# Kernel tuning notes

Measured on AMD Instinct MI355X. Metric: run time of the kernel, lower is better.

## Reference

```python
import jax, jax.numpy as jnp
import numpy as np

N_NODES = 100000
N_EDGES = 1600000
IN_DIM, HIDDEN, OUT = 256, 128, 64


def setup_inputs() -> dict:
    key = jax.random.key(0)
    k1, k2, k3, k4 = jax.random.split(key, 4)
    x = jax.random.normal(k1, (N_NODES, IN_DIM), dtype=jnp.float32)
    edge_index = jax.random.randint(k2, (2, N_EDGES), 0, N_NODES, dtype=jnp.int32)
    # glorot-ish init for the GCN linear layers
    W1 = jax.random.normal(k3, (IN_DIM, HIDDEN), dtype=jnp.float32) / np.sqrt(IN_DIM)
    b1 = jnp.zeros((HIDDEN,), dtype=jnp.float32)
    W2 = jax.random.normal(k4, (HIDDEN, OUT), dtype=jnp.float32) / np.sqrt(HIDDEN)
    b2 = jnp.zeros((OUT,), dtype=jnp.float32)
    return {"x": x, "edge_index": edge_index, "W1": W1, "b1": b1, "W2": W2, "b2": b2}


def gcn_layer(x, src, dst, W, b):
    """PyG GCNConv: add self-loops, symmetric deg^-1/2 normalization,
    linear transform, scatter-add aggregation, bias."""
    h = x @ W  # [N, F_out]
    # degree over self-looped graph: in-degree(dst counts) + 1 self loop
    deg = jax.ops.segment_sum(jnp.ones((src.shape[0],), h.dtype), dst,
                              num_segments=N_NODES) + 1.0
    dinv = jax.lax.rsqrt(deg)  # [N]
    coef = dinv[src] * dinv[dst]  # [E]
    agg = jax.ops.segment_sum(h[src] * coef[:, None], dst, num_segments=N_NODES)
    # self-loop contribution (norm = dinv[i]^2) without materializing loop edges
    agg = agg + h * (dinv * dinv)[:, None]
    return agg + b


def reference(x, edge_index, W1, b1, W2, b2):
    src, dst = edge_index[0], edge_index[1]
    h = jax.nn.relu(gcn_layer(x, src, dst, W1, b1))
    return jax.nn.relu(gcn_layer(h, src, dst, W2, b2))
```

## Files before the change

### kernel.cpp

```cpp
#include <hip/hip_runtime.h>

#define N_NODES 100000
#define N_EDGES 1600000
#define IN_DIM 256
#define HIDDEN 128
#define OUT_DIM 64
#define LDA 40

#define NBIN 391
#define NBLK3 256
#define CHUNK 6250
#define NMAT (NBIN * NBLK3)
#define NBLK_SCAN (NMAT / 256)
#define CAP 6144

typedef __bf16 bf16x8 __attribute__((ext_vector_type(8)));
typedef __bf16 bf16x4 __attribute__((ext_vector_type(4)));
typedef float f32x4 __attribute__((ext_vector_type(4)));

__launch_bounds__(256)
__global__ void k_hist(const int* __restrict__ dst, int* __restrict__ cnt2) {
    __shared__ int hist[NBIN];
    for (int i = threadIdx.x; i < NBIN; i += 256) hist[i] = 0;
    __syncthreads();
    int base = blockIdx.x * CHUNK;
    for (int i = threadIdx.x; i < CHUNK; i += 256)
        atomicAdd(&hist[dst[base + i] >> 8], 1);
    __syncthreads();
    for (int k = threadIdx.x; k < NBIN; k += 256)
        cnt2[k * NBLK3 + blockIdx.x] = hist[k];
}

__global__ void k_scan1(int* __restrict__ a, int* __restrict__ bsum) {
    __shared__ int tmp[256];
    int t = threadIdx.x;
    int i = blockIdx.x * 256 + t;
    int v = a[i];
    tmp[t] = v;
    __syncthreads();
    #pragma unroll
    for (int off = 1; off < 256; off <<= 1) {
        int p = (t >= off) ? tmp[t - off] : 0;
        __syncthreads();
        tmp[t] += p;
        __syncthreads();
    }
    a[i] = tmp[t] - v;
    if (t == 255) bsum[blockIdx.x] = tmp[255];
}

__global__ void k_scan2(int* __restrict__ bsum) {
    __shared__ int tmp[512];
    int t = threadIdx.x;
    int v = (t < NBLK_SCAN) ? bsum[t] : 0;
    tmp[t] = v;
    __syncthreads();
    #pragma unroll
    for (int off = 1; off < 512; off <<= 1) {
        int p = (t >= off) ? tmp[t - off] : 0;
        __syncthreads();
        tmp[t] += p;
        __syncthreads();
    }
    if (t < NBLK_SCAN) bsum[t] = tmp[t] - v;
}

__global__ void k_scan3(int* __restrict__ a, const int* __restrict__ bsum) {
    int i = blockIdx.x * 256 + threadIdx.x;
    a[i] += bsum[blockIdx.x];
}

__launch_bounds__(256)
__global__ void k_scatter_bins(const int* __restrict__ src, const int* __restrict__ dst,
                               const int* __restrict__ off2,
                               unsigned int* __restrict__ ebuf) {
    __shared__ int cursor[NBIN];
    for (int k = threadIdx.x; k < NBIN; k += 256)
        cursor[k] = off2[k * NBLK3 + blockIdx.x];
    __syncthreads();
    int base = blockIdx.x * CHUNK;
    for (int i = threadIdx.x; i < CHUNK; i += 256) {
        int s = src[base + i], d = dst[base + i];
        int pos = atomicAdd(&cursor[d >> 8], 1);
        ebuf[pos] = ((unsigned)s << 8) | (unsigned)(d & 255);
    }
}

__launch_bounds__(256)
__global__ void k_fine(const unsigned int* __restrict__ ebuf, const int* __restrict__ off2,
                       int* __restrict__ esrc, int* __restrict__ rowstart,
                       float* __restrict__ dinv) {
    __shared__ int hist[256];
    __shared__ int tmp[256];
    __shared__ int nodeoff[256];
    __shared__ int cursor[256];
    __shared__ unsigned int ed[CAP];
    __shared__ int sOut[CAP];

    const int k = blockIdx.x;
    const int t = threadIdx.x;
    const int e0 = off2[k * NBLK3];
    const int e1 = (k + 1 < NBIN) ? off2[(k + 1) * NBLK3] : N_EDGES;
    int m = e1 - e0;
    if (m > CAP) m = CAP;

    hist[t] = 0;
    __syncthreads();
    for (int i = t; i < m; i += 256) {
        unsigned v = ebuf[e0 + i];
        ed[i] = v;
        atomicAdd(&hist[v & 255], 1);
    }
    __syncthreads();

    int v = hist[t];
    tmp[t] = v;
    __syncthreads();
    #pragma unroll
    for (int off = 1; off < 256; off <<= 1) {
        int p = (t >= off) ? tmp[t - off] : 0;
        __syncthreads();
        tmp[t] += p;
        __syncthreads();
    }
    nodeoff[t] = tmp[t] - v;
    cursor[t] = tmp[t] - v;
    __syncthreads();

    for (int i = t; i < m; i += 256) {
        unsigned e = ed[i];
        int pos = atomicAdd(&cursor[e & 255], 1);
        sOut[pos] = (int)(e >> 8);
    }
    __syncthreads();

    for (int i = t; i < m; i += 256) esrc[e0 + i] = sOut[i];

    int n = k * 256 + t;
    if (n < N_NODES) {
        rowstart[n] = e0 + nodeoff[t];
        dinv[n] = rsqrtf((float)hist[t] + 1.0f);
    }
    if (k == 0 && t == 0) rowstart[N_NODES] = N_EDGES;
}

__launch_bounds__(256, 2)
__global__ void k_gemm1(const float* __restrict__ X, const float* __restrict__ W1,
                        __bf16* __restrict__ H) {
    __shared__ __attribute__((aligned(16))) __bf16 As[128 * LDA];
    __shared__ __attribute__((aligned(16))) __bf16 Bs[128 * LDA];

    const int t = threadIdx.x;
    const int wave = t >> 6;
    const int lane = t & 63;
    const int wr = wave >> 1, wc = wave & 1;
    const int lm = lane & 15;
    const int q = lane >> 4;
    const int row0 = blockIdx.x * 128;

    f32x4 acc[4][4] = {};

    for (int k0 = 0; k0 < IN_DIM; k0 += 32) {
        #pragma unroll
        for (int p = 0; p < 4; ++p) {
            int r = p * 32 + (t >> 3);
            int kk = (t & 7) * 4;
            int g = row0 + r;
            float4 v = make_float4(0.f, 0.f, 0.f, 0.f);
            if (g < N_NODES) v = *(const float4*)&X[g * IN_DIM + k0 + kk];
            __bf16* dp = &As[r * LDA + kk];
            dp[0] = (__bf16)v.x; dp[1] = (__bf16)v.y;
            dp[2] = (__bf16)v.z; dp[3] = (__bf16)v.w;
        }
        #pragma unroll
        for (int p = 0; p < 4; ++p) {
            int idx = p * 256 + t;
            int kk = idx >> 5;
            int c = (idx & 31) * 4;
            float4 v = *(const float4*)&W1[(k0 + kk) * HIDDEN + c];
            Bs[(c + 0) * LDA + kk] = (__bf16)v.x;
            Bs[(c + 1) * LDA + kk] = (__bf16)v.y;
            Bs[(c + 2) * LDA + kk] = (__bf16)v.z;
            Bs[(c + 3) * LDA + kk] = (__bf16)v.w;
        }
        __syncthreads();

        bf16x8 af[4], bfr[4];
        #pragma unroll
        for (int mi = 0; mi < 4; ++mi)
            af[mi] = *(const bf16x8*)&As[(wr * 64 + mi * 16 + lm) * LDA + q * 8];
        #pragma unroll
        for (int ni = 0; ni < 4; ++ni)
            bfr[ni] = *(const bf16x8*)&Bs[(wc * 64 + ni * 16 + lm) * LDA + q * 8];
        #pragma unroll
        for (int mi = 0; mi < 4; ++mi)
            #pragma unroll
            for (int ni = 0; ni < 4; ++ni)
                acc[mi][ni] = __builtin_amdgcn_mfma_f32_16x16x32_bf16(
                    af[mi], bfr[ni], acc[mi][ni], 0, 0, 0);
        __syncthreads();
    }

    #pragma unroll
    for (int mi = 0; mi < 4; ++mi) {
        #pragma unroll
        for (int r = 0; r < 4; ++r) {
            int grow = row0 + wr * 64 + mi * 16 + q * 4 + r;
            if (grow < N_NODES) {
                #pragma unroll
                for (int ni = 0; ni < 4; ++ni) {
                    int col = wc * 64 + ni * 16 + lm;
                    H[grow * HIDDEN + col] = (__bf16)acc[mi][ni][r];
                }
            }
        }
    }
}

__launch_bounds__(256)
__global__ void k_gather1(const int* __restrict__ rowstart, const int* __restrict__ esrc,
                          const float* __restrict__ dinv,
                          const __bf16* __restrict__ H, const float* __restrict__ b1,
                          __bf16* __restrict__ AGG) {
    int n = blockIdx.x * 16 + (threadIdx.x >> 4);
    if (n >= N_NODES) return;
    int j = (threadIdx.x & 15) * 8;

    float dn = dinv[n];
    float s = dn * dn;
    bf16x8 h = *(const bf16x8*)&H[n * HIDDEN + j];
    float acc[8];
    #pragma unroll
    for (int i = 0; i < 8; ++i) acc[i] = (float)h[i] * s;

    int p0 = rowstart[n], p1 = rowstart[n + 1];
    int p = p0;
    for (; p + 3 < p1; p += 4) {
        int s0 = esrc[p + 0], s1 = esrc[p + 1], s2 = esrc[p + 2], s3 = esrc[p + 3];
        float c0 = dinv[s0] * dn, c1 = dinv[s1] * dn;
        float c2 = dinv[s2] * dn, c3 = dinv[s3] * dn;
        bf16x8 v0 = *(const bf16x8*)&H[s0 * HIDDEN + j];
        bf16x8 v1 = *(const bf16x8*)&H[s1 * HIDDEN + j];
        bf16x8 v2 = *(const bf16x8*)&H[s2 * HIDDEN + j];
        bf16x8 v3 = *(const bf16x8*)&H[s3 * HIDDEN + j];
        #pragma unroll
        for (int i = 0; i < 8; ++i) acc[i] = fmaf((float)v0[i], c0, acc[i]);
        #pragma unroll
        for (int i = 0; i < 8; ++i) acc[i] = fmaf((float)v1[i], c1, acc[i]);
        #pragma unroll
        for (int i = 0; i < 8; ++i) acc[i] = fmaf((float)v2[i], c2, acc[i]);
        #pragma unroll
        for (int i = 0; i < 8; ++i) acc[i] = fmaf((float)v3[i], c3, acc[i]);
    }
    for (; p < p1; ++p) {
        int sidx = esrc[p];
        float c = dinv[sidx] * dn;
        bf16x8 v = *(const bf16x8*)&H[sidx * HIDDEN + j];
        #pragma unroll
        for (int i = 0; i < 8; ++i) acc[i] = fmaf((float)v[i], c, acc[i]);
    }

    float4 bb0 = *(const float4*)&b1[j];
    float4 bb1 = *(const float4*)&b1[j + 4];
    bf16x8 o;
    o[0] = (__bf16)fmaxf(acc[0] + bb0.x, 0.f);
    o[1] = (__bf16)fmaxf(acc[1] + bb0.y, 0.f);
    o[2] = (__bf16)fmaxf(acc[2] + bb0.z, 0.f);
    o[3] = (__bf16)fmaxf(acc[3] + bb0.w, 0.f);
    o[4] = (__bf16)fmaxf(acc[4] + bb1.x, 0.f);
    o[5] = (__bf16)fmaxf(acc[5] + bb1.y, 0.f);
    o[6] = (__bf16)fmaxf(acc[6] + bb1.z, 0.f);
    o[7] = (__bf16)fmaxf(acc[7] + bb1.w, 0.f);
    *(bf16x8*)&AGG[n * HIDDEN + j] = o;
}

__launch_bounds__(256, 2)
__global__ void k_gemm2(const __bf16* __restrict__ AGG, const float* __restrict__ W2,
                        __bf16* __restrict__ H2) {
    __shared__ __attribute__((aligned(16))) __bf16 As[128 * LDA];
    __shared__ __attribute__((aligned(16))) __bf16 Bs[64 * LDA];

    const int t = threadIdx.x;
    const int wave = t >> 6;
    const int lane = t & 63;
    const int lm = lane & 15;
    const int q = lane >> 4;
    const int row0 = blockIdx.x * 128;

    f32x4 acc[2][4] = {};

    for (int k0 = 0; k0 < HIDDEN; k0 += 32) {
        #pragma unroll
        for (int p = 0; p < 2; ++p) {
            int idx = p * 256 + t;
            int r = idx >> 2;
            int seg = (idx & 3) * 8;
            int g = row0 + r;
            uint4 v = make_uint4(0u, 0u, 0u, 0u);
            if (g < N_NODES) v = *(const uint4*)&AGG[g * HIDDEN + k0 + seg];
            *(uint4*)&As[r * LDA + seg] = v;
        }
        #pragma unroll
        for (int p = 0; p < 2; ++p) {
            int idx = p * 256 + t;
            int kk = idx >> 4;
            int c = (idx & 15) * 4;
            float4 v = *(const float4*)&W2[(k0 + kk) * OUT_DIM + c];
            Bs[(c + 0) * LDA + kk] = (__bf16)v.x;
            Bs[(c + 1) * LDA + kk] = (__bf16)v.y;
            Bs[(c + 2) * LDA + kk] = (__bf16)v.z;
            Bs[(c + 3) * LDA + kk] = (__bf16)v.w;
        }
        __syncthreads();

        bf16x8 af[2], bfr[4];
        #pragma unroll
        for (int mi = 0; mi < 2; ++mi)
            af[mi] = *(const bf16x8*)&As[(wave * 32 + mi * 16 + lm) * LDA + q * 8];
        #pragma unroll
        for (int ni = 0; ni < 4; ++ni)
            bfr[ni] = *(const bf16x8*)&Bs[(ni * 16 + lm) * LDA + q * 8];
        #pragma unroll
        for (int mi = 0; mi < 2; ++mi)
            #pragma unroll
            for (int ni = 0; ni < 4; ++ni)
                acc[mi][ni] = __builtin_amdgcn_mfma_f32_16x16x32_bf16(
                    af[mi], bfr[ni], acc[mi][ni], 0, 0, 0);
        __syncthreads();
    }

    #pragma unroll
    for (int mi = 0; mi < 2; ++mi) {
        #pragma unroll
        for (int r = 0; r < 4; ++r) {
            int grow = row0 + wave * 32 + mi * 16 + q * 4 + r;
            if (grow < N_NODES) {
                #pragma unroll
                for (int ni = 0; ni < 4; ++ni) {
                    int col = ni * 16 + lm;
                    H2[grow * OUT_DIM + col] = (__bf16)acc[mi][ni][r];
                }
            }
        }
    }
}

__launch_bounds__(256)
__global__ void k_gather2(const int* __restrict__ rowstart, const int* __restrict__ esrc,
                          const float* __restrict__ dinv,
                          const __bf16* __restrict__ H2, const float* __restrict__ b2,
                          float* __restrict__ OUT) {
    int n = blockIdx.x * 32 + (threadIdx.x >> 3);
    if (n >= N_NODES) return;
    int j = (threadIdx.x & 7) * 8;

    float dn = dinv[n];
    float s = dn * dn;
    bf16x8 h = *(const bf16x8*)&H2[n * OUT_DIM + j];
    float acc[8];
    #pragma unroll
    for (int i = 0; i < 8; ++i) acc[i] = (float)h[i] * s;

    int p0 = rowstart[n], p1 = rowstart[n + 1];
    int p = p0;
    for (; p + 3 < p1; p += 4) {
        int s0 = esrc[p + 0], s1 = esrc[p + 1], s2 = esrc[p + 2], s3 = esrc[p + 3];
        float c0 = dinv[s0] * dn, c1 = dinv[s1] * dn;
        float c2 = dinv[s2] * dn, c3 = dinv[s3] * dn;
        bf16x8 v0 = *(const bf16x8*)&H2[s0 * OUT_DIM + j];
        bf16x8 v1 = *(const bf16x8*)&H2[s1 * OUT_DIM + j];
        bf16x8 v2 = *(const bf16x8*)&H2[s2 * OUT_DIM + j];
        bf16x8 v3 = *(const bf16x8*)&H2[s3 * OUT_DIM + j];
        #pragma unroll
        for (int i = 0; i < 8; ++i) acc[i] = fmaf((float)v0[i], c0, acc[i]);
        #pragma unroll
        for (int i = 0; i < 8; ++i) acc[i] = fmaf((float)v1[i], c1, acc[i]);
        #pragma unroll
        for (int i = 0; i < 8; ++i) acc[i] = fmaf((float)v2[i], c2, acc[i]);
        #pragma unroll
        for (int i = 0; i < 8; ++i) acc[i] = fmaf((float)v3[i], c3, acc[i]);
    }
    for (; p < p1; ++p) {
        int sidx = esrc[p];
        float c = dinv[sidx] * dn;
        bf16x8 v = *(const bf16x8*)&H2[sidx * OUT_DIM + j];
        #pragma unroll
        for (int i = 0; i < 8; ++i) acc[i] = fmaf((float)v[i], c, acc[i]);
    }

    float4 bb0 = *(const float4*)&b2[j];
    float4 bb1 = *(const float4*)&b2[j + 4];
    float4 o0, o1;
    o0.x = fmaxf(acc[0] + bb0.x, 0.f);
    o0.y = fmaxf(acc[1] + bb0.y, 0.f);
    o0.z = fmaxf(acc[2] + bb0.z, 0.f);
    o0.w = fmaxf(acc[3] + bb0.w, 0.f);
    o1.x = fmaxf(acc[4] + bb1.x, 0.f);
    o1.y = fmaxf(acc[5] + bb1.y, 0.f);
    o1.z = fmaxf(acc[6] + bb1.z, 0.f);
    o1.w = fmaxf(acc[7] + bb1.w, 0.f);
    *(float4*)&OUT[n * OUT_DIM + j] = o0;
    *(float4*)&OUT[n * OUT_DIM + j + 4] = o1;
}

extern "C" void kernel_launch(void* const* d_in, const int* in_sizes, int n_in,
                              void* d_out, int out_size, void* d_ws, size_t ws_size,
                              hipStream_t stream) {
    const float* x  = (const float*)d_in[0];
    const int* ei   = (const int*)d_in[1];
    const float* W1 = (const float*)d_in[2];
    const float* b1 = (const float*)d_in[3];
    const float* W2 = (const float*)d_in[4];
    const float* b2 = (const float*)d_in[5];
    float* out = (float*)d_out;

    const int* src = ei;
    const int* dst = ei + N_EDGES;

    char* ws = (char*)d_ws;
    int*          cnt2     = (int*)         (ws + 0x000000);
    int*          bsum     = (int*)         (ws + 0x080000);
    int*          rowstart = (int*)         (ws + 0x090000);
    float*        dinv     = (float*)       (ws + 0x100000);
    unsigned int* ebuf     = (unsigned int*)(ws + 0x180000);
    int*          esrc     = (int*)         (ws + 0x800000);
    __bf16*       h1       = (__bf16*)      (ws + 0xE80000);
    __bf16*       agg1     = (__bf16*)      (ws + 0x2880000);
    __bf16*       h2       = (__bf16*)      (ws + 0x4280000);

    k_hist<<<NBLK3, 256, 0, stream>>>(dst, cnt2);
    k_scan1<<<NBLK_SCAN, 256, 0, stream>>>(cnt2, bsum);
    k_scan2<<<1, 512, 0, stream>>>(bsum);
    k_scan3<<<NBLK_SCAN, 256, 0, stream>>>(cnt2, bsum);
    k_scatter_bins<<<NBLK3, 256, 0, stream>>>(src, dst, cnt2, ebuf);
    k_fine<<<NBIN, 256, 0, stream>>>(ebuf, cnt2, esrc, rowstart, dinv);

    k_gemm1<<<(N_NODES + 127) / 128, 256, 0, stream>>>(x, W1, h1);
    k_gather1<<<(N_NODES + 15) / 16, 256, 0, stream>>>(rowstart, esrc, dinv, h1, b1, agg1);
    k_gemm2<<<(N_NODES + 127) / 128, 256, 0, stream>>>(agg1, W2, h2);
    k_gather2<<<(N_NODES + 31) / 32, 256, 0, stream>>>(rowstart, esrc, dinv, h2, b2, out);
}
```

Measured before the change: 347.4 us.

## Preload whole weight matrix into swizzled LDS and stream A fragments directly from global

Result: slower. 365.4 us (+5.2%).

```diff
diff --git a/kernel.cpp b/kernel.cpp
--- a/kernel.cpp
+++ b/kernel.cpp
@@ -5,7 +5,6 @@
 #define IN_DIM 256
 #define HIDDEN 128
 #define OUT_DIM 64
-#define LDA 40
 
 #define NBIN 391
 #define NBLK3 256
@@ -144,74 +143,73 @@
     if (k == 0 && t == 0) rowstart[N_NODES] = N_EDGES;
 }
 
+__device__ __forceinline__ int bsw1(int c, int kk) {
+    return c * 256 + (kk ^ ((c & 7) << 3));
+}
+
 __launch_bounds__(256, 2)
 __global__ void k_gemm1(const float* __restrict__ X, const float* __restrict__ W1,
                         __bf16* __restrict__ H) {
-    __shared__ __attribute__((aligned(16))) __bf16 As[128 * LDA];
-    __shared__ __attribute__((aligned(16))) __bf16 Bs[128 * LDA];
+    __shared__ __attribute__((aligned(16))) __bf16 Bs[128 * 256];
 
     const int t = threadIdx.x;
     const int wave = t >> 6;
     const int lane = t & 63;
-    const int wr = wave >> 1, wc = wave & 1;
     const int lm = lane & 15;
     const int q = lane >> 4;
     const int row0 = blockIdx.x * 128;
 
-    f32x4 acc[4][4] = {};
-
+    for (int i = t; i < 256 * 32; i += 256) {
+        int kk = i >> 5;
+        int c4 = (i & 31) * 4;
+        float4 v = *(const float4*)&W1[kk * HIDDEN + c4];
+        Bs[bsw1(c4 + 0, kk)] = (__bf16)v.x;
+        Bs[bsw1(c4 + 1, kk)] = (__bf16)v.y;
+        Bs[bsw1(c4 + 2, kk)] = (__bf16)v.z;
+        Bs[bsw1(c4 + 3, kk)] = (__bf16)v.w;
+    }
+    __syncthreads();
+
+    f32x4 acc[2][8] = {};
+
+    #pragma unroll
     for (int k0 = 0; k0 < IN_DIM; k0 += 32) {
-        #pragma unroll
-        for (int p = 0; p < 4; ++p) {
-            int r = p * 32 + (t >> 3);
-            int kk = (t & 7) * 4;
-            int g = row0 + r;
-            float4 v = make_float4(0.f, 0.f, 0.f, 0.f);
-            if (g < N_NODES) v = *(const float4*)&X[g * IN_DIM + k0 + kk];
-            __bf16* dp = &As[r * LDA + kk];
-            dp[0] = (__bf16)v.x; dp[1] = (__bf16)v.y;
-            dp[2] = (__bf16)v.z; dp[3] = (__bf16)v.w;
-        }
-        #pragma unroll
-        for (int p = 0; p < 4; ++p) {
-            int idx = p * 256 + t;
-            int kk = idx >> 5;
-            int c = (idx & 31) * 4;
-            float4 v = *(const float4*)&W1[(k0 + kk) * HIDDEN + c];
-            Bs[(c + 0) * LDA + kk] = (__bf16)v.x;
-            Bs[(c + 1) * LDA + kk] = (__bf16)v.y;
-            Bs[(c + 2) * LDA + kk] = (__bf16)v.z;
-            Bs[(c + 3) * LDA + kk] = (__bf16)v.w;
-        }
-        __syncthreads();
-
-        bf16x8 af[4], bfr[4];
-        #pragma unroll
-        for (int mi = 0; mi < 4; ++mi)
-            af[mi] = *(const bf16x8*)&As[(wr * 64 + mi * 16 + lm) * LDA + q * 8];
-        #pragma unroll
-        for (int ni = 0; ni < 4; ++ni)
-            bfr[ni] = *(const bf16x8*)&Bs[(wc * 64 + ni * 16 + lm) * LDA + q * 8];
-        #pragma unroll
-        for (int mi = 0; mi < 4; ++mi)
+        bf16x8 af[2];
+        #pragma unroll
+        for (int mi = 0; mi < 2; ++mi) {
+            int g = row0 + wave * 32 + mi * 16 + lm;
+            float4 v0 = make_float4(0.f, 0.f, 0.f, 0.f), v1 = v0;
+            if (g < N_NODES) {
+                const float* p = &X[(size_t)g * IN_DIM + k0 + q * 8];
+                v0 = *(const float4*)p;
+                v1 = *(const float4*)(p + 4);
+            }
+            bf16x8 a;
+            a[0] = (__bf16)v0.x; a[1] = (__bf16)v0.y;
+            a[2] = (__bf16)v0.z; a[3] = (__bf16)v0.w;
+            a[4] = (__bf16)v1.x; a[5] = (__bf16)v1.y;
+            a[6] = (__bf16)v1.z; a[7] = (__bf16)v1.w;
+            af[mi] = a;
+        }
+        #pragma unroll
+        for (int ni = 0; ni < 8; ++ni) {
+            bf16x8 bfr = *(const bf16x8*)&Bs[bsw1(ni * 16 + lm, k0 + q * 8)];
             #pragma unroll
-            for (int ni = 0; ni < 4; ++ni)
+            for (int mi = 0; mi < 2; ++mi)
                 acc[mi][ni] = __builtin_amdgcn_mfma_f32_16x16x32_bf16(
-                    af[mi], bfr[ni], acc[mi][ni], 0, 0, 0);
-        __syncthreads();
-    }
-
-    #pragma unroll
-    for (int mi = 0; mi < 4; ++mi) {
+                    af[mi], bfr, acc[mi][ni], 0, 0, 0);
+        }
+    }
+
+    #pragma unroll
+    for (int mi = 0; mi < 2; ++mi) {
         #pragma unroll
         for (int r = 0; r < 4; ++r) {
-            int grow = row0 + wr * 64 + mi * 16 + q * 4 + r;
+            int grow = row0 + wave * 32 + mi * 16 + q * 4 + r;
             if (grow < N_NODES) {
                 #pragma unroll
-                for (int ni = 0; ni < 4; ++ni) {
-                    int col = wc * 64 + ni * 16 + lm;
-                    H[grow * HIDDEN + col] = (__bf16)acc[mi][ni][r];
-                }
+                for (int ni = 0; ni < 8; ++ni)
+                    H[grow * HIDDEN + ni * 16 + lm] = (__bf16)acc[mi][ni][r];
             }
         }
     }
@@ -274,11 +272,14 @@
     *(bf16x8*)&AGG[n * HIDDEN + j] = o;
 }
 
+__device__ __forceinline__ int bsw2(int c, int kk) {
+    return c * 128 + (kk ^ ((c & 7) << 3));
+}
+
 __launch_bounds__(256, 2)
 __global__ void k_gemm2(const __bf16* __restrict__ AGG, const float* __restrict__ W2,
                         __bf16* __restrict__ H2) {
-    __shared__ __attribute__((aligned(16))) __bf16 As[128 * LDA];
-    __shared__ __attribute__((aligned(16))) __bf16 Bs[64 * LDA];
+    __shared__ __attribute__((aligned(16))) __bf16 Bs[64 * 128];
 
     const int t = threadIdx.x;
     const int wave = t >> 6;
@@ -287,46 +288,38 @@
     const int q = lane >> 4;
     const int row0 = blockIdx.x * 128;
 
+    for (int i = t; i < 128 * 16; i += 256) {
+        int kk = i >> 4;
+        int c4 = (i & 15) * 4;
+        float4 v = *(const float4*)&W2[kk * OUT_DIM + c4];
+        Bs[bsw2(c4 + 0, kk)] = (__bf16)v.x;
+        Bs[bsw2(c4 + 1, kk)] = (__bf16)v.y;
+        Bs[bsw2(c4 + 2, kk)] = (__bf16)v.z;
+        Bs[bsw2(c4 + 3, kk)] = (__bf16)v.w;
+    }
+    __syncthreads();
+
     f32x4 acc[2][4] = {};
 
+    #pragma unroll
     for (int k0 = 0; k0 < HIDDEN; k0 += 32) {
-        #pragma unroll
-        for (int p = 0; p < 2; ++p) {
-            int idx = p * 256 + t;
-            int r = idx >> 2;
-            int seg = (idx & 3) * 8;
-            int g = row0 + r;
-            uint4 v = make_uint4(0u, 0u, 0u, 0u);
-            if (g < N_NODES) v = *(const uint4*)&AGG[g * HIDDEN + k0 + seg];
-            *(uint4*)&As[r * LDA + seg] = v;
-        }
-        #pragma unroll
-        for (int p = 0; p < 2; ++p) {
-            int idx = p * 256 + t;
-            int kk = idx >> 4;
-            int c = (idx & 15) * 4;
-            float4 v = *(const float4*)&W2[(k0 + kk) * OUT_DIM + c];
-            Bs[(c + 0) * LDA + kk] = (__bf16)v.x;
-            Bs[(c + 1) * LDA + kk] = (__bf16)v.y;
-            Bs[(c + 2) * LDA + kk] = (__bf16)v.z;
-            Bs[(c + 3) * LDA + kk] = (__bf16)v.w;
-        }
-        __syncthreads();
-
-        bf16x8 af[2], bfr[4];
-        #pragma unroll
-        for (int mi = 0; mi < 2; ++mi)
-            af[mi] = *(const bf16x8*)&As[(wave * 32 + mi * 16 + lm) * LDA + q * 8];
-        #pragma unroll
-        for (int ni = 0; ni < 4; ++ni)
-            bfr[ni] = *(const bf16x8*)&Bs[(ni * 16 + lm) * LDA + q * 8];
-        #pragma unroll
-        for (int mi = 0; mi < 2; ++mi)
+        bf16x8 af[2];
+        #pragma unroll
+        for (int mi = 0; mi < 2; ++mi) {
+            int g = row0 + wave * 32 + mi * 16 + lm;
+            bf16x8 a = {};
+            if (g < N_NODES)
+                a = *(const bf16x8*)&AGG[(size_t)g * HIDDEN + k0 + q * 8];
+            af[mi] = a;
+        }
+        #pragma unroll
+        for (int ni = 0; ni < 4; ++ni) {
+            bf16x8 bfr = *(const bf16x8*)&Bs[bsw2(ni * 16 + lm, k0 + q * 8)];
             #pragma unroll
-            for (int ni = 0; ni < 4; ++ni)
+            for (int mi = 0; mi < 2; ++mi)
                 acc[mi][ni] = __builtin_amdgcn_mfma_f32_16x16x32_bf16(
-                    af[mi], bfr[ni], acc[mi][ni], 0, 0, 0);
-        __syncthreads();
+                    af[mi], bfr, acc[mi][ni], 0, 0, 0);
+        }
     }
 
     #pragma unroll
@@ -336,10 +329,8 @@
             int grow = row0 + wave * 32 + mi * 16 + q * 4 + r;
             if (grow < N_NODES) {
                 #pragma unroll
-                for (int ni = 0; ni < 4; ++ni) {
-                    int col = ni * 16 + lm;
-                    H2[grow * OUT_DIM + col] = (__bf16)acc[mi][ni][r];
-                }
+                for (int ni = 0; ni < 4; ++ni)
+                    H2[grow * OUT_DIM + ni * 16 + lm] = (__bf16)acc[mi][ni][r];
             }
         }
     }
```
